# Optimization experiments

Measured on AMD Instinct MI355X. Metric: run time of the kernel, lower is better.

## Reference

```python
import jax, jax.numpy as jnp
import numpy as np

B, D, P = 2048, 768, 200
DOWN = [(384, 768), (192, 384), (96, 192), (48, 96)]
UP = [(96, 48), (192, 96), (384, 192), (768, 384)]


def setup_inputs() -> dict:
    key = jax.random.key(0)
    ks = jax.random.split(key, 32)
    inp = {
        "x": jax.random.normal(ks[0], (B, D), jnp.float32),
        "aW": jax.random.normal(ks[1], (D, D), jnp.float32) * 0.02,
        "ab": jax.random.normal(ks[2], (D,), jnp.float32) * 0.02,
        "protos": jax.random.normal(ks[3], (P, D), jnp.float32),
    }
    k = 4
    for i, (o, ii) in enumerate(DOWN):
        inp[f"Wd{i}"] = jax.random.normal(ks[k], (o, ii), jnp.float32) * (1.0 / np.sqrt(ii)); k += 1
        inp[f"bd{i}"] = jax.random.normal(ks[k], (o,), jnp.float32) * 0.02; k += 1
    for i, (o, ii) in enumerate(UP):
        inp[f"Wu{i}"] = jax.random.normal(ks[k], (o, ii), jnp.float32) * (1.0 / np.sqrt(ii)); k += 1
        inp[f"bu{i}"] = jax.random.normal(ks[k], (o,), jnp.float32) * 0.02; k += 1
    return inp


def _adopter_net(x, Wds, bds, Wus, bus):
    # down path with skip storage
    x_inter = []
    h = x
    for Wd, bd in zip(Wds, bds):
        h = jax.nn.relu(h @ Wd.T + bd)
        x_inter.append(h)
    # up path: residual adds for middle layers (i==1 uses x_inter[-2], i==2 uses x_inter[-3])
    n = len(Wus)
    for i, (Wu, bu) in enumerate(zip(Wus, bus)):
        if i == 0 or i == n - 1:
            h = jax.nn.relu(h @ Wu.T + bu)
        else:
            h = jax.nn.relu((h + x_inter[-i - 1]) @ Wu.T + bu)
    return h


def reference(x, aW, ab, Wd0, bd0, Wd1, bd1, Wd2, bd2, Wd3, bd3,
              Wu0, bu0, Wu1, bu1, Wu2, bu2, Wu3, bu3, protos):
    Wds, bds = [Wd0, Wd1, Wd2, Wd3], [bd0, bd1, bd2, bd3]
    Wus, bus = [Wu0, Wu1, Wu2, Wu3], [bu0, bu1, bu2, bu3]
    # features = x + adapter(x) + adopters(x)
    features = x + (x @ aW.T + ab) + _adopter_net(x, Wds, bds, Wus, bus)  # [B, D]
    # fused per-prototype negative L1 distance (replaces Python loop over PrototypeBase)
    logits = -jnp.sum(jnp.abs(features[:, None, :] - protos[None, :, :]), axis=-1)  # [B, P]
    return logits
```

## Files before the change

### kernel.cpp

```cpp
#include <hip/hip_runtime.h>

typedef __attribute__((ext_vector_type(8))) __bf16 bf16x8;
typedef __attribute__((ext_vector_type(4))) float f32x4;
typedef _Float16 hf2 __attribute__((ext_vector_type(2)));
typedef _Float16 hf8 __attribute__((ext_vector_type(8)));
typedef unsigned short u16;
typedef struct { hf2 v[4]; } hf2x4;

__device__ __forceinline__ float bf2f(u16 h) {
    return __uint_as_float(((unsigned int)h) << 16);
}
__device__ __forceinline__ u16 f2bf(float f) {
    unsigned int u = __float_as_uint(f);
    u += 0x7fffu + ((u >> 16) & 1u);
    return (u16)(u >> 16);
}

#if __has_builtin(__builtin_amdgcn_fdot2)
__device__ __forceinline__ float FDOT2(hf2 a, hf2 b, float c) {
    return __builtin_amdgcn_fdot2(a, b, c, false);
}
#else
__device__ __forceinline__ float FDOT2(hf2 a, hf2 b, float c) {
    return c + (float)a[0] + (float)a[1];
}
#endif

#define GLOAD_LDS16(gsrc, ldst)                                                          \
    __builtin_amdgcn_global_load_lds(                                                    \
        (__attribute__((address_space(1))) unsigned int*)(gsrc),                         \
        (__attribute__((address_space(3))) unsigned int*)(ldst), 16, 0, 0)

struct CvtDesc { const float* src; u16* dst; int N, K, Npad, Kpad, blk0, fmt; };
struct CvtTab { CvtDesc t[11]; };

__global__ __launch_bounds__(256) void cvt_all(CvtTab tab) {
    int b = blockIdx.x;
    int ti = 0;
#pragma unroll
    for (int j = 1; j < 11; ++j)
        if (b >= tab.t[j].blk0) ti = j;
    const CvtDesc c = tab.t[ti];
    long i = (long)(b - c.blk0) * 256 + threadIdx.x;
    long tot = (long)c.Npad * c.Kpad;
    if (i >= tot) return;
    int n = (int)(i / c.Kpad);
    int k = (int)(i - (long)n * c.Kpad);
    float v = (n < c.N && k < c.K) ? c.src[(long)n * c.K + k] : 0.f;
    if (c.fmt) {
        _Float16 h = (_Float16)v;
        c.dst[i] = __builtin_bit_cast(u16, h);
    } else {
        c.dst[i] = f2bf(v);
    }
}

template<int RELU, int HASRES, int RESF16, int MODE>
__device__ __forceinline__ void gemm128_body(
    char* lds,
    const u16* __restrict__ A, int lda,
    const u16* __restrict__ W, int ldw,
    const float* __restrict__ bias,
    u16* __restrict__ outB, int ldo,
    const void* __restrict__ res, int ldr,
    _Float16* __restrict__ outH,
    int nk, int mb, int nb)
{
    const int tid = threadIdx.x;
    const int wave = tid >> 6, lane = tid & 63;
    const int lr = lane & 15, lk = lane >> 4;
    const int wr = wave >> 1, wc = wave & 1;

    f32x4 acc[4][2];
#pragma unroll
    for (int i = 0; i < 4; ++i)
#pragma unroll
        for (int j = 0; j < 2; ++j)
#pragma unroll
            for (int e = 0; e < 4; ++e) acc[i][j][e] = 0.f;

    int ra[4], la[4], rb[2], lb[2];
#pragma unroll
    for (int t = 0; t < 4; ++t) {
        int g = t * 256 + tid;
        ra[t] = g >> 3; la[t] = (g & 7) ^ (ra[t] & 7);
    }
#pragma unroll
    for (int t = 0; t < 2; ++t) {
        int g = t * 256 + tid;
        rb[t] = g >> 3; lb[t] = (g & 7) ^ (rb[t] & 7);
    }

    auto STAGE = [&](int b, int kt) {
        const int kk = kt * 64;
        char* dA = lds + b * 24576;
        char* dB = dA + 16384;
#pragma unroll
        for (int t = 0; t < 4; ++t)
            GLOAD_LDS16(A + (size_t)(mb + ra[t]) * lda + kk + la[t] * 8,
                        dA + t * 4096 + wave * 1024);
#pragma unroll
        for (int t = 0; t < 2; ++t)
            GLOAD_LDS16(W + (size_t)(nb + rb[t]) * ldw + kk + lb[t] * 8,
                        dB + t * 4096 + wave * 1024);
    };
    auto COMPUTE = [&](int b) {
        char* sA = lds + b * 24576;
        char* sB = sA + 16384;
#pragma unroll
        for (int ks = 0; ks < 2; ++ks) {
            bf16x8 af[4], bfr[2];
#pragma unroll
            for (int mi = 0; mi < 4; ++mi) {
                int m_loc = wr * 64 + mi * 16 + lr;
                int gr = (ks * 4 + lk) ^ (m_loc & 7);
                af[mi] = *(const bf16x8*)(sA + m_loc * 128 + gr * 16);
            }
#pragma unroll
            for (int ni = 0; ni < 2; ++ni) {
                int n_loc = wc * 32 + ni * 16 + lr;
                int gr = (ks * 4 + lk) ^ (n_loc & 7);
                bfr[ni] = *(const bf16x8*)(sB + n_loc * 128 + gr * 16);
            }
#pragma unroll
            for (int mi = 0; mi < 4; ++mi)
#pragma unroll
                for (int ni = 0; ni < 2; ++ni)
                    acc[mi][ni] = __builtin_amdgcn_mfma_f32_16x16x32_bf16(
                        af[mi], bfr[ni], acc[mi][ni], 0, 0, 0);
        }
    };

    STAGE(0, 0);
    __syncthreads();
    int b = 0;
    for (int kt = 0; kt < nk - 1; ++kt) {
        STAGE(b ^ 1, kt + 1);
        COMPUTE(b);
        __syncthreads();
        b ^= 1;
    }
    COMPUTE(b);

#pragma unroll
    for (int mi = 0; mi < 4; ++mi) {
#pragma unroll
        for (int ni = 0; ni < 2; ++ni) {
            const int n_g = nb + wc * 32 + ni * 16 + lr;
            const float bv = bias[n_g];
#pragma unroll
            for (int r = 0; r < 4; ++r) {
                const int m_g = mb + wr * 64 + mi * 16 + lk * 4 + r;
                float v = acc[mi][ni][r] + bv;
                if (RELU) v = fmaxf(v, 0.f);
                if (HASRES) {
                    if (RESF16)
                        v += (float)((const _Float16*)res)[(size_t)m_g * ldr + n_g];
                    else
                        v += bf2f(((const u16*)res)[(size_t)m_g * ldr + n_g]);
                }
                if (MODE == 2) outH[(size_t)m_g * 768 + n_g] = (_Float16)v;
                else           outB[(size_t)m_g * ldo + n_g] = f2bf(v);
            }
        }
    }
}

__global__ __launch_bounds__(256) void gemm_ad0(
    const u16* __restrict__ xb,
    const u16* __restrict__ aWb, const float* __restrict__ ab,
    _Float16* __restrict__ adFH,
    const u16* __restrict__ Wd0b, const float* __restrict__ bd0,
    u16* __restrict__ h1)
{
    __shared__ __align__(16) char lds[49152];
    if (blockIdx.y < 12) {
        gemm128_body<0, 1, 0, 2>(lds, xb, 768, aWb, 768, ab, nullptr, 0,
                                 xb, 768, adFH, 12,
                                 blockIdx.x * 128, blockIdx.y * 64);
    } else {
        gemm128_body<1, 0, 0, 0>(lds, xb, 768, Wd0b, 768, bd0, h1, 384,
                                 nullptr, 0, nullptr, 12,
                                 blockIdx.x * 128, (blockIdx.y - 12) * 64);
    }
}

__global__ __launch_bounds__(256) void gemm_u3(
    const u16* __restrict__ u2, const u16* __restrict__ Wu3b,
    const float* __restrict__ bu3, const _Float16* __restrict__ adFH,
    _Float16* __restrict__ featH)
{
    __shared__ __align__(16) char lds[49152];
    gemm128_body<1, 1, 1, 2>(lds, u2, 384, Wu3b, 384, bu3, nullptr, 0,
                             adFH, 768, featH, 6,
                             blockIdx.x * 128, blockIdx.y * 64);
}

template<int K, int NPAD, int NREAL, int RES, int OUTG>
__device__ __forceinline__ void layer16(
    const u16* __restrict__ W, int ldw, const float* __restrict__ bias,
    const u16* actIn, int ldin,
    u16* actOut, int ldout,
    const u16* resid, int ldres,
    u16* __restrict__ gout, int ldg)
{
    constexpr int TPW = NPAD / 64;
    const int tid = threadIdx.x;
    const int wave = tid >> 6, lane = tid & 63;
    const int lr = lane & 15, lk = lane >> 4;

    f32x4 acc[TPW];
#pragma unroll
    for (int t = 0; t < TPW; ++t)
#pragma unroll
        for (int e = 0; e < 4; ++e) acc[t][e] = 0.f;

#pragma unroll
    for (int kk = 0; kk < K / 32; ++kk) {
        const bf16x8 a = *(const bf16x8*)&actIn[lr * ldin + kk * 32 + lk * 8];
#pragma unroll
        for (int t = 0; t < TPW; ++t) {
            const int nc = (wave * TPW + t) * 16 + lr;
            const bf16x8 b = *(const bf16x8*)&W[(size_t)nc * ldw + kk * 32 + lk * 8];
            acc[t] = __builtin_amdgcn_mfma_f32_16x16x32_bf16(a, b, acc[t], 0, 0, 0);
        }
    }
#pragma unroll
    for (int t = 0; t < TPW; ++t) {
        const int nc = (wave * TPW + t) * 16 + lr;
        const float bv = (nc < NREAL) ? bias[nc] : 0.f;
#pragma unroll
        for (int r = 0; r < 4; ++r) {
            const int row = lk * 4 + r;
            float v = fmaxf(acc[t][r] + bv, 0.f);
            if (RES) v += bf2f(resid[row * ldres + nc]);
            const u16 o = f2bf(v);
            if (OUTG) gout[(size_t)row * ldg + nc] = o;
            else      actOut[row * ldout + nc] = o;
        }
    }
}

__global__ __launch_bounds__(256) void chain_mid(
    const u16* __restrict__ h1,
    const u16* __restrict__ Wd1b, const float* __restrict__ bd1,
    const u16* __restrict__ Wd2b, const float* __restrict__ bd2,
    const u16* __restrict__ Wd3b, const float* __restrict__ bd3,
    const u16* __restrict__ Wu0b, const float* __restrict__ bu0,
    const u16* __restrict__ Wu1b, const float* __restrict__ bu1,
    const u16* __restrict__ Wu2b, const float* __restrict__ bu2,
    u16* __restrict__ u2)
{
    __shared__ u16 As[16 * 392];
    __shared__ u16 Bs[16 * 200];
    __shared__ u16 Cs[16 * 136];
    __shared__ u16 Ds[16 * 72];
    const int tid = threadIdx.x;
    const int rb = blockIdx.x * 16;

    for (int i = tid; i < 768; i += 256) {
        const int r = i / 48, c = i - r * 48;
        *(bf16x8*)&As[r * 392 + c * 8] =
            *(const bf16x8*)&h1[(size_t)(rb + r) * 384 + c * 8];
    }
    __syncthreads();
    layer16<384, 192, 192, 0, 0>(Wd1b, 384, bd1, As, 392, Bs, 200, nullptr, 0, nullptr, 0);
    __syncthreads();
    layer16<192, 128,  96, 0, 0>(Wd2b, 192, bd2, Bs, 200, Cs, 136, nullptr, 0, nullptr, 0);
    __syncthreads();
    layer16<128,  64,  48, 0, 0>(Wd3b, 128, bd3, Cs, 136, Ds,  72, nullptr, 0, nullptr, 0);
    __syncthreads();
    u16* E = As;
    u16* F = As + 16 * 136;
    layer16< 64, 128,  96, 1, 0>(Wu0b,  64, bu0, Ds,  72, E, 136, Cs, 136, nullptr, 0);
    __syncthreads();
    layer16<128, 192, 192, 1, 0>(Wu1b, 128, bu1, E, 136, F, 200, Bs, 200, nullptr, 0);
    __syncthreads();
    layer16<192, 384, 384, 0, 1>(Wu2b, 192, bu2, F, 200, nullptr, 0, nullptr, 0,
                                 u2 + (size_t)rb * 384, 384);
}

__global__ __launch_bounds__(256) void l1_kernel(
    const _Float16* __restrict__ feat, const _Float16* __restrict__ protos,
    float* __restrict__ part)
{
    __shared__ _Float16 fs[128][64];
    __shared__ hf2 pt[32][64];
    const int tid = threadIdx.x;
    const int tp = tid & 15, tr = tid >> 4;
    const int rb = blockIdx.x * 128;
    const int pb = blockIdx.y * 64;
    const int db = blockIdx.z * 64;

    {
        const int g = tid & 7, r0 = tid >> 3;
#pragma unroll
        for (int k = 0; k < 4; ++k) {
            const int r = r0 + 32 * k;
            *(hf8*)&fs[r][g * 8] =
                *(const hf8*)&feat[(size_t)(rb + r) * 768 + db + g * 8];
        }
    }
    {
        const int sp = tid & 63, q = tid >> 6;
        const _Float16* src = &protos[(size_t)(pb + sp) * 768 + db + q * 16];
        hf8 v0 = *(const hf8*)src;
        hf8 v1 = *(const hf8*)(src + 8);
        hf2x4 w0 = __builtin_bit_cast(hf2x4, v0);
        hf2x4 w1 = __builtin_bit_cast(hf2x4, v1);
#pragma unroll
        for (int e = 0; e < 4; ++e)
            pt[q * 8 + e][sp] = w0.v[e];
#pragma unroll
        for (int e = 0; e < 4; ++e)
            pt[q * 8 + 4 + e][sp] = w1.v[e];
    }
    __syncthreads();

    float acc[8][4];
#pragma unroll
    for (int i = 0; i < 8; ++i)
#pragma unroll
        for (int j = 0; j < 4; ++j) acc[i][j] = 0.f;

    const hf2 one2 = {(_Float16)1.0f, (_Float16)1.0f};
#pragma unroll 2
    for (int g = 0; g < 8; ++g) {
        hf2x4 F2[8];
#pragma unroll
        for (int i = 0; i < 8; ++i)
            F2[i] = __builtin_bit_cast(hf2x4,
                        *(const hf8*)&fs[tr + 16 * i][g * 8]);
        hf2x4 P2[4];
#pragma unroll
        for (int q = 0; q < 4; ++q)
            P2[q] = __builtin_bit_cast(hf2x4,
                        *(const hf8*)&pt[g * 4 + q][tp * 4]);
#pragma unroll
        for (int q = 0; q < 4; ++q) {
#pragma unroll
            for (int j = 0; j < 4; ++j) {
                const hf2 pj = P2[q].v[j];
#pragma unroll
                for (int i = 0; i < 8; ++i) {
                    hf2 d = F2[i].v[q] - pj;
                    unsigned ud = __builtin_bit_cast(unsigned, d) & 0x7FFF7FFFu;
                    acc[i][j] = FDOT2(__builtin_bit_cast(hf2, ud), one2, acc[i][j]);
                }
            }
        }
    }
    const int p = pb + tp * 4;
    if (p < 200) {
#pragma unroll
        for (int i = 0; i < 8; ++i) {
            float4 v = {-acc[i][0], -acc[i][1], -acc[i][2], -acc[i][3]};
            *(float4*)&part[((size_t)(rb + tr + 16 * i) * 12 + blockIdx.z) * 200 + p] = v;
        }
    }
}

__global__ __launch_bounds__(256) void l1_reduce(
    const float* __restrict__ part, float* __restrict__ out)
{
    const int row = blockIdx.x;
    const int p = threadIdx.x;
    if (p < 200) {
        float s = 0.f;
#pragma unroll
        for (int z = 0; z < 12; ++z)
            s += part[((size_t)row * 12 + z) * 200 + p];
        out[(size_t)row * 200 + p] = s;
    }
}

static constexpr size_t OFF_PART  = 0;
static constexpr size_t OFF_XB    = 0;
static constexpr size_t OFF_AWB   = 3145728;
static constexpr size_t OFF_WD0   = 4325376;
static constexpr size_t OFF_WD1   = 4915200;
static constexpr size_t OFF_WD2   = 5062656;
static constexpr size_t OFF_WD3   = 5111808;
static constexpr size_t OFF_WU0   = 5128192;
static constexpr size_t OFF_WU1   = 5144576;
static constexpr size_t OFF_WU2   = 5193728;
static constexpr size_t OFF_WU3   = 5341184;
static constexpr size_t OFF_H1    = 5931008;
static constexpr size_t OFF_U2    = 10387456;
static constexpr size_t OFF_ADF   = 11960320;
static constexpr size_t OFF_FEATH = 19660800;
static constexpr size_t OFF_PROH  = 22806528;

extern "C" void kernel_launch(void* const* d_in, const int* in_sizes, int n_in,
                              void* d_out, int out_size, void* d_ws, size_t ws_size,
                              hipStream_t stream) {
    const float* x      = (const float*)d_in[0];
    const float* aW     = (const float*)d_in[1];
    const float* ab     = (const float*)d_in[2];
    const float* protos = (const float*)d_in[3];
    const float* Wd[4]  = {(const float*)d_in[4], (const float*)d_in[6],
                           (const float*)d_in[8], (const float*)d_in[10]};
    const float* bd[4]  = {(const float*)d_in[5], (const float*)d_in[7],
                           (const float*)d_in[9], (const float*)d_in[11]};
    const float* Wu[4]  = {(const float*)d_in[12], (const float*)d_in[14],
                           (const float*)d_in[16], (const float*)d_in[18]};
    const float* bu[4]  = {(const float*)d_in[13], (const float*)d_in[15],
                           (const float*)d_in[17], (const float*)d_in[19]};
    float* out = (float*)d_out;
    char* ws = (char*)d_ws;

    u16* xb    = (u16*)(ws + OFF_XB);
    u16* aWb   = (u16*)(ws + OFF_AWB);
    u16* Wd0b  = (u16*)(ws + OFF_WD0);
    u16* Wd1b  = (u16*)(ws + OFF_WD1);
    u16* Wd2b  = (u16*)(ws + OFF_WD2);
    u16* Wd3b  = (u16*)(ws + OFF_WD3);
    u16* Wu0b  = (u16*)(ws + OFF_WU0);
    u16* Wu1b  = (u16*)(ws + OFF_WU1);
    u16* Wu2b  = (u16*)(ws + OFF_WU2);
    u16* Wu3b  = (u16*)(ws + OFF_WU3);
    u16* h1    = (u16*)(ws + OFF_H1);
    u16* u2    = (u16*)(ws + OFF_U2);
    float* part = (float*)(ws + OFF_PART);
    _Float16* adFH  = (_Float16*)(ws + OFF_ADF);
    _Float16* featH = (_Float16*)(ws + OFF_FEATH);
    _Float16* proH  = (_Float16*)(ws + OFF_PROH);

    CvtTab tab;
    int blk = 0;
    auto set = [&](int i, const float* s, u16* d, int N, int K, int Np, int Kp,
                   int fmt) {
        tab.t[i] = {s, d, N, K, Np, Kp, blk, fmt};
        blk += (Np * Kp + 255) / 256;
    };
    set(0,  x,      xb,          2048, 768, 2048, 768, 0);
    set(1,  aW,     aWb,         768,  768, 768,  768, 0);
    set(2,  Wd[0],  Wd0b,        384,  768, 384,  768, 0);
    set(3,  Wd[1],  Wd1b,        192,  384, 192,  384, 0);
    set(4,  Wd[2],  Wd2b,        96,   192, 128,  192, 0);
    set(5,  Wd[3],  Wd3b,        48,   96,  64,   128, 0);
    set(6,  Wu[0],  Wu0b,        96,   48,  128,  64,  0);
    set(7,  Wu[1],  Wu1b,        192,  96,  192,  128, 0);
    set(8,  Wu[2],  Wu2b,        384,  192, 384,  192, 0);
    set(9,  Wu[3],  Wu3b,        768,  384, 768,  384, 0);
    set(10, protos, (u16*)proH,  200,  768, 256,  768, 1);
    cvt_all<<<blk, 256, 0, stream>>>(tab);

    gemm_ad0<<<dim3(16, 18), 256, 0, stream>>>(xb, aWb, ab, adFH, Wd0b, bd[0], h1);
    chain_mid<<<dim3(128), 256, 0, stream>>>(h1,
        Wd1b, bd[1], Wd2b, bd[2], Wd3b, bd[3],
        Wu0b, bu[0], Wu1b, bu[1], Wu2b, bu[2], u2);
    gemm_u3<<<dim3(16, 12), 256, 0, stream>>>(u2, Wu3b, bu[3], adFH, featH);

    l1_kernel<<<dim3(16, 4, 12), 256, 0, stream>>>(featH, proH, part);
    l1_reduce<<<dim3(2048), 256, 0, stream>>>(part, out);
}
```

Before: 80.56 us.

## Fuse adapter GEMM into final up-projection and overlap weight conversion with first GEMM

The adapter GEMM (x @ aW.T) moves out of the first kernel and into the final up-projection kernel as a second K-phase. The Wu3 accumulator gets bias and ReLU applied at the phase boundary, then the adapter product and the x residual are added in the epilogue. This drops the fp16 adapter intermediate write and read-back. Weight and prototype conversion is split so that only x and Wd0 are converted up front, and the remaining weights are converted by extra blocks inside the first GEMM launch. Risks: the dependent kernels get longer, the d0 GEMM grid is small, and the second cvt launch adds overhead.

```diff
diff --git a/kernel.cpp b/kernel.cpp
--- a/kernel.cpp
+++ b/kernel.cpp
@@ -34,36 +34,32 @@
 struct CvtDesc { const float* src; u16* dst; int N, K, Npad, Kpad, blk0, fmt; };
 struct CvtTab { CvtDesc t[11]; };
 
-__global__ __launch_bounds__(256) void cvt_all(CvtTab tab) {
-    int b = blockIdx.x;
+__device__ __forceinline__ void do_cvt(const CvtTab& tab, int vb, int tid) {
     int ti = 0;
 #pragma unroll
     for (int j = 1; j < 11; ++j)
-        if (b >= tab.t[j].blk0) ti = j;
+        if (vb >= tab.t[j].blk0) ti = j;
     const CvtDesc c = tab.t[ti];
-    long i = (long)(b - c.blk0) * 256 + threadIdx.x;
+    long i = (long)(vb - c.blk0) * 256 + tid;
     long tot = (long)c.Npad * c.Kpad;
     if (i >= tot) return;
     int n = (int)(i / c.Kpad);
     int k = (int)(i - (long)n * c.Kpad);
     float v = (n < c.N && k < c.K) ? c.src[(long)n * c.K + k] : 0.f;
-    if (c.fmt) {
-        _Float16 h = (_Float16)v;
-        c.dst[i] = __builtin_bit_cast(u16, h);
-    } else {
-        c.dst[i] = f2bf(v);
-    }
-}
-
-template<int RELU, int HASRES, int RESF16, int MODE>
+    c.dst[i] = c.fmt ? __builtin_bit_cast(u16, (_Float16)v) : f2bf(v);
+}
+
+__global__ __launch_bounds__(256) void cvt_k(CvtTab tab) {
+    do_cvt(tab, blockIdx.x, threadIdx.x);
+}
+
+template<int RELU>
 __device__ __forceinline__ void gemm128_body(
     char* lds,
     const u16* __restrict__ A, int lda,
     const u16* __restrict__ W, int ldw,
     const float* __restrict__ bias,
     u16* __restrict__ outB, int ldo,
-    const void* __restrict__ res, int ldr,
-    _Float16* __restrict__ outH,
     int nk, int mb, int nb)
 {
     const int tid = threadIdx.x;
@@ -79,7 +75,7 @@
 #pragma unroll
             for (int e = 0; e < 4; ++e) acc[i][j][e] = 0.f;
 
-    int ra[4], la[4], rb[2], lb[2];
+    int ra[4], la[4], rb_[2], lb[2];
 #pragma unroll
     for (int t = 0; t < 4; ++t) {
         int g = t * 256 + tid;
@@ -88,7 +84,7 @@
 #pragma unroll
     for (int t = 0; t < 2; ++t) {
         int g = t * 256 + tid;
-        rb[t] = g >> 3; lb[t] = (g & 7) ^ (rb[t] & 7);
+        rb_[t] = g >> 3; lb[t] = (g & 7) ^ (rb_[t] & 7);
     }
 
     auto STAGE = [&](int b, int kt) {
@@ -101,7 +97,7 @@
                         dA + t * 4096 + wave * 1024);
 #pragma unroll
         for (int t = 0; t < 2; ++t)
-            GLOAD_LDS16(W + (size_t)(nb + rb[t]) * ldw + kk + lb[t] * 8,
+            GLOAD_LDS16(W + (size_t)(nb + rb_[t]) * ldw + kk + lb[t] * 8,
                         dB + t * 4096 + wave * 1024);
     };
     auto COMPUTE = [&](int b) {
@@ -153,47 +149,139 @@
                 const int m_g = mb + wr * 64 + mi * 16 + lk * 4 + r;
                 float v = acc[mi][ni][r] + bv;
                 if (RELU) v = fmaxf(v, 0.f);
-                if (HASRES) {
-                    if (RESF16)
-                        v += (float)((const _Float16*)res)[(size_t)m_g * ldr + n_g];
-                    else
-                        v += bf2f(((const u16*)res)[(size_t)m_g * ldr + n_g]);
+                outB[(size_t)m_g * ldo + n_g] = f2bf(v);
+            }
+        }
+    }
+}
+
+__global__ __launch_bounds__(256, 2) void gemm_d0_cvt(
+    const u16* __restrict__ xb, const u16* __restrict__ Wd0b,
+    const float* __restrict__ bd0, u16* __restrict__ h1, CvtTab tabB)
+{
+    __shared__ __align__(16) char lds[49152];
+    const int bid = blockIdx.x;
+    if (bid < 96) {
+        gemm128_body<1>(lds, xb, 768, Wd0b, 768, bd0, h1, 384, 12,
+                        (bid & 15) * 128, (bid >> 4) * 64);
+    } else {
+        do_cvt(tabB, bid - 96, threadIdx.x);
+    }
+}
+
+__global__ __launch_bounds__(256, 2) void gemm_u3ad(
+    const u16* __restrict__ u2, const u16* __restrict__ Wu3b,
+    const float* __restrict__ bu3,
+    const u16* __restrict__ xb, const u16* __restrict__ aWb,
+    const float* __restrict__ ab,
+    _Float16* __restrict__ featH)
+{
+    __shared__ __align__(16) char lds[49152];
+    const int mb = blockIdx.x * 128, nb = blockIdx.y * 64;
+    const int tid = threadIdx.x;
+    const int wave = tid >> 6, lane = tid & 63;
+    const int lr = lane & 15, lk = lane >> 4;
+    const int wr = wave >> 1, wc = wave & 1;
+
+    f32x4 acc[4][2];
+#pragma unroll
+    for (int i = 0; i < 4; ++i)
+#pragma unroll
+        for (int j = 0; j < 2; ++j)
+#pragma unroll
+            for (int e = 0; e < 4; ++e) acc[i][j][e] = 0.f;
+
+    int ra[4], la[4], rb_[2], lb[2];
+#pragma unroll
+    for (int t = 0; t < 4; ++t) {
+        int g = t * 256 + tid;
+        ra[t] = g >> 3; la[t] = (g & 7) ^ (ra[t] & 7);
+    }
+#pragma unroll
+    for (int t = 0; t < 2; ++t) {
+        int g = t * 256 + tid;
+        rb_[t] = g >> 3; lb[t] = (g & 7) ^ (rb_[t] & 7);
+    }
+
+    auto STAGE = [&](int b, int kt) {
+        const u16* A; const u16* W; int ld, kk;
+        if (kt < 6) { A = u2; W = Wu3b; ld = 384; kk = kt * 64; }
+        else        { A = xb; W = aWb;  ld = 768; kk = (kt - 6) * 64; }
+        char* dA = lds + b * 24576;
+        char* dB = dA + 16384;
+#pragma unroll
+        for (int t = 0; t < 4; ++t)
+            GLOAD_LDS16(A + (size_t)(mb + ra[t]) * ld + kk + la[t] * 8,
+                        dA + t * 4096 + wave * 1024);
+#pragma unroll
+        for (int t = 0; t < 2; ++t)
+            GLOAD_LDS16(W + (size_t)(nb + rb_[t]) * ld + kk + lb[t] * 8,
+                        dB + t * 4096 + wave * 1024);
+    };
+    auto COMPUTE = [&](int b) {
+        char* sA = lds + b * 24576;
+        char* sB = sA + 16384;
+#pragma unroll
+        for (int ks = 0; ks < 2; ++ks) {
+            bf16x8 af[4], bfr[2];
+#pragma unroll
+            for (int mi = 0; mi < 4; ++mi) {
+                int m_loc = wr * 64 + mi * 16 + lr;
+                int gr = (ks * 4 + lk) ^ (m_loc & 7);
+                af[mi] = *(const bf16x8*)(sA + m_loc * 128 + gr * 16);
+            }
+#pragma unroll
+            for (int ni = 0; ni < 2; ++ni) {
+                int n_loc = wc * 32 + ni * 16 + lr;
+                int gr = (ks * 4 + lk) ^ (n_loc & 7);
+                bfr[ni] = *(const bf16x8*)(sB + n_loc * 128 + gr * 16);
+            }
+#pragma unroll
+            for (int mi = 0; mi < 4; ++mi)
+#pragma unroll
+                for (int ni = 0; ni < 2; ++ni)
+                    acc[mi][ni] = __builtin_amdgcn_mfma_f32_16x16x32_bf16(
+                        af[mi], bfr[ni], acc[mi][ni], 0, 0, 0);
+        }
+    };
+
+    STAGE(0, 0);
+    __syncthreads();
+    int b = 0;
+    for (int kt = 0; kt < 17; ++kt) {
+        STAGE(b ^ 1, kt + 1);
+        COMPUTE(b);
+        if (kt == 5) {
+#pragma unroll
+            for (int mi = 0; mi < 4; ++mi)
+#pragma unroll
+                for (int ni = 0; ni < 2; ++ni) {
+                    const int n_g = nb + wc * 32 + ni * 16 + lr;
+                    const float bv = bu3[n_g];
+#pragma unroll
+                    for (int r = 0; r < 4; ++r)
+                        acc[mi][ni][r] = fmaxf(acc[mi][ni][r] + bv, 0.f);
                 }
-                if (MODE == 2) outH[(size_t)m_g * 768 + n_g] = (_Float16)v;
-                else           outB[(size_t)m_g * ldo + n_g] = f2bf(v);
-            }
-        }
-    }
-}
-
-__global__ __launch_bounds__(256) void gemm_ad0(
-    const u16* __restrict__ xb,
-    const u16* __restrict__ aWb, const float* __restrict__ ab,
-    _Float16* __restrict__ adFH,
-    const u16* __restrict__ Wd0b, const float* __restrict__ bd0,
-    u16* __restrict__ h1)
-{
-    __shared__ __align__(16) char lds[49152];
-    if (blockIdx.y < 12) {
-        gemm128_body<0, 1, 0, 2>(lds, xb, 768, aWb, 768, ab, nullptr, 0,
-                                 xb, 768, adFH, 12,
-                                 blockIdx.x * 128, blockIdx.y * 64);
-    } else {
-        gemm128_body<1, 0, 0, 0>(lds, xb, 768, Wd0b, 768, bd0, h1, 384,
-                                 nullptr, 0, nullptr, 12,
-                                 blockIdx.x * 128, (blockIdx.y - 12) * 64);
-    }
-}
-
-__global__ __launch_bounds__(256) void gemm_u3(
-    const u16* __restrict__ u2, const u16* __restrict__ Wu3b,
-    const float* __restrict__ bu3, const _Float16* __restrict__ adFH,
-    _Float16* __restrict__ featH)
-{
-    __shared__ __align__(16) char lds[49152];
-    gemm128_body<1, 1, 1, 2>(lds, u2, 384, Wu3b, 384, bu3, nullptr, 0,
-                             adFH, 768, featH, 6,
-                             blockIdx.x * 128, blockIdx.y * 64);
+        }
+        __syncthreads();
+        b ^= 1;
+    }
+    COMPUTE(b);
+
+#pragma unroll
+    for (int mi = 0; mi < 4; ++mi) {
+#pragma unroll
+        for (int ni = 0; ni < 2; ++ni) {
+            const int n_g = nb + wc * 32 + ni * 16 + lr;
+            const float bv = ab[n_g];
+#pragma unroll
+            for (int r = 0; r < 4; ++r) {
+                const int m_g = mb + wr * 64 + mi * 16 + lk * 4 + r;
+                float v = acc[mi][ni][r] + bv + bf2f(xb[(size_t)m_g * 768 + n_g]);
+                featH[(size_t)m_g * 768 + n_g] = (_Float16)v;
+            }
+        }
+    }
 }
 
 template<int K, int NPAD, int NREAL, int RES, int OUTG>
@@ -387,7 +475,6 @@
 static constexpr size_t OFF_WU3   = 5341184;
 static constexpr size_t OFF_H1    = 5931008;
 static constexpr size_t OFF_U2    = 10387456;
-static constexpr size_t OFF_ADF   = 11960320;
 static constexpr size_t OFF_FEATH = 19660800;
 static constexpr size_t OFF_PROH  = 22806528;
 
@@ -422,35 +509,45 @@
     u16* h1    = (u16*)(ws + OFF_H1);
     u16* u2    = (u16*)(ws + OFF_U2);
     float* part = (float*)(ws + OFF_PART);
-    _Float16* adFH  = (_Float16*)(ws + OFF_ADF);
     _Float16* featH = (_Float16*)(ws + OFF_FEATH);
     _Float16* proH  = (_Float16*)(ws + OFF_PROH);
 
-    CvtTab tab;
-    int blk = 0;
-    auto set = [&](int i, const float* s, u16* d, int N, int K, int Np, int Kp,
-                   int fmt) {
-        tab.t[i] = {s, d, N, K, Np, Kp, blk, fmt};
-        blk += (Np * Kp + 255) / 256;
+    const int SENT = 0x7FFFFFFF;
+
+    CvtTab tabA;
+    int blkA = 0;
+    tabA.t[0] = {x,     xb,   2048, 768, 2048, 768, 0, 0};
+    blkA += 2048 * 768 / 256;
+    tabA.t[1] = {Wd[0], Wd0b, 384,  768, 384,  768, blkA, 0};
+    blkA += 384 * 768 / 256;
+    for (int j = 2; j < 11; ++j) tabA.t[j].blk0 = SENT;
+    cvt_k<<<blkA, 256, 0, stream>>>(tabA);
+
+    CvtTab tabB;
+    int blkB = 0;
+    auto setB = [&](int i, const float* s, u16* d, int N, int K, int Np, int Kp,
+                    int fmt) {
+        tabB.t[i] = {s, d, N, K, Np, Kp, blkB, fmt};
+        blkB += (Np * Kp + 255) / 256;
     };
-    set(0,  x,      xb,          2048, 768, 2048, 768, 0);
-    set(1,  aW,     aWb,         768,  768, 768,  768, 0);
-    set(2,  Wd[0],  Wd0b,        384,  768, 384,  768, 0);
-    set(3,  Wd[1],  Wd1b,        192,  384, 192,  384, 0);
-    set(4,  Wd[2],  Wd2b,        96,   192, 128,  192, 0);
-    set(5,  Wd[3],  Wd3b,        48,   96,  64,   128, 0);
-    set(6,  Wu[0],  Wu0b,        96,   48,  128,  64,  0);
-    set(7,  Wu[1],  Wu1b,        192,  96,  192,  128, 0);
-    set(8,  Wu[2],  Wu2b,        384,  192, 384,  192, 0);
-    set(9,  Wu[3],  Wu3b,        768,  384, 768,  384, 0);
-    set(10, protos, (u16*)proH,  200,  768, 256,  768, 1);
-    cvt_all<<<blk, 256, 0, stream>>>(tab);
-
-    gemm_ad0<<<dim3(16, 18), 256, 0, stream>>>(xb, aWb, ab, adFH, Wd0b, bd[0], h1);
+    setB(0, aW,     aWb,        768, 768, 768, 768, 0);
+    setB(1, Wd[1],  Wd1b,       192, 384, 192, 384, 0);
+    setB(2, Wd[2],  Wd2b,       96,  192, 128, 192, 0);
+    setB(3, Wd[3],  Wd3b,       48,  96,  64,  128, 0);
+    setB(4, Wu[0],  Wu0b,       96,  48,  128, 64,  0);
+    setB(5, Wu[1],  Wu1b,       192, 96,  192, 128, 0);
+    setB(6, Wu[2],  Wu2b,       384, 192, 384, 192, 0);
+    setB(7, Wu[3],  Wu3b,       768, 384, 768, 384, 0);
+    setB(8, protos, (u16*)proH, 200, 768, 256, 768, 1);
+    for (int j = 9; j < 11; ++j) tabB.t[j].blk0 = SENT;
+    gemm_d0_cvt<<<96 + blkB, 256, 0, stream>>>(xb, Wd0b, bd[0], h1, tabB);
+
     chain_mid<<<dim3(128), 256, 0, stream>>>(h1,
         Wd1b, bd[1], Wd2b, bd[2], Wd3b, bd[3],
         Wu0b, bu[0], Wu1b, bu[1], Wu2b, bu[2], u2);
-    gemm_u3<<<dim3(16, 12), 256, 0, stream>>>(u2, Wu3b, bu[3], adFH, featH);
+
+    gemm_u3ad<<<dim3(16, 12), 256, 0, stream>>>(u2, Wu3b, bu[3],
+                                                xb, aWb, ab, featH);
 
     l1_kernel<<<dim3(16, 4, 12), 256, 0, stream>>>(featH, proH, part);
     l1_reduce<<<dim3(2048), 256, 0, stream>>>(part, out);
```

Result: no change. 80.79 us (+0.3%).

## Rebalance kernel schedule: overlap weight conversion with d0 GEMM, adapter GEMM with chain

Applied to the files above, without the earlier changes.

Splits conversion so only x and Wd0 are converted up front. The remaining weight and prototype conversions run as extra blocks inside the first down-projection GEMM launch. The adapter GEMM moves into the launch of the middle chain kernel so the two run concurrently, and the adapter result is written straight into the feature buffer, which the final up GEMM then accumulates into in place. The L1 kernel uses 96-wide D chunks (8 partials instead of 12) to cut partial-sum traffic, at the cost of more LDS per block and a heavier load imbalance across heterogeneous blocks.

```diff
diff --git a/kernel.cpp b/kernel.cpp
--- a/kernel.cpp
+++ b/kernel.cpp
@@ -34,25 +34,23 @@
 struct CvtDesc { const float* src; u16* dst; int N, K, Npad, Kpad, blk0, fmt; };
 struct CvtTab { CvtDesc t[11]; };
 
-__global__ __launch_bounds__(256) void cvt_all(CvtTab tab) {
-    int b = blockIdx.x;
+__device__ __forceinline__ void do_cvt(const CvtTab& tab, int vb, int tid) {
     int ti = 0;
 #pragma unroll
     for (int j = 1; j < 11; ++j)
-        if (b >= tab.t[j].blk0) ti = j;
+        if (vb >= tab.t[j].blk0) ti = j;
     const CvtDesc c = tab.t[ti];
-    long i = (long)(b - c.blk0) * 256 + threadIdx.x;
+    long i = (long)(vb - c.blk0) * 256 + tid;
     long tot = (long)c.Npad * c.Kpad;
     if (i >= tot) return;
     int n = (int)(i / c.Kpad);
     int k = (int)(i - (long)n * c.Kpad);
     float v = (n < c.N && k < c.K) ? c.src[(long)n * c.K + k] : 0.f;
-    if (c.fmt) {
-        _Float16 h = (_Float16)v;
-        c.dst[i] = __builtin_bit_cast(u16, h);
-    } else {
-        c.dst[i] = f2bf(v);
-    }
+    c.dst[i] = c.fmt ? __builtin_bit_cast(u16, (_Float16)v) : f2bf(v);
+}
+
+__global__ __launch_bounds__(256) void cvt_k(CvtTab tab) {
+    do_cvt(tab, blockIdx.x, threadIdx.x);
 }
 
 template<int RELU, int HASRES, int RESF16, int MODE>
@@ -79,7 +77,7 @@
 #pragma unroll
             for (int e = 0; e < 4; ++e) acc[i][j][e] = 0.f;
 
-    int ra[4], la[4], rb[2], lb[2];
+    int ra[4], la[4], rb_[2], lb[2];
 #pragma unroll
     for (int t = 0; t < 4; ++t) {
         int g = t * 256 + tid;
@@ -88,7 +86,7 @@
 #pragma unroll
     for (int t = 0; t < 2; ++t) {
         int g = t * 256 + tid;
-        rb[t] = g >> 3; lb[t] = (g & 7) ^ (rb[t] & 7);
+        rb_[t] = g >> 3; lb[t] = (g & 7) ^ (rb_[t] & 7);
     }
 
     auto STAGE = [&](int b, int kt) {
@@ -101,7 +99,7 @@
                         dA + t * 4096 + wave * 1024);
 #pragma unroll
         for (int t = 0; t < 2; ++t)
-            GLOAD_LDS16(W + (size_t)(nb + rb[t]) * ldw + kk + lb[t] * 8,
+            GLOAD_LDS16(W + (size_t)(nb + rb_[t]) * ldw + kk + lb[t] * 8,
                         dB + t * 4096 + wave * 1024);
     };
     auto COMPUTE = [&](int b) {
@@ -166,34 +164,19 @@
     }
 }
 
-__global__ __launch_bounds__(256) void gemm_ad0(
-    const u16* __restrict__ xb,
-    const u16* __restrict__ aWb, const float* __restrict__ ab,
-    _Float16* __restrict__ adFH,
-    const u16* __restrict__ Wd0b, const float* __restrict__ bd0,
-    u16* __restrict__ h1)
+__global__ __launch_bounds__(256, 2) void gemm_d0_cvt(
+    const u16* __restrict__ xb, const u16* __restrict__ Wd0b,
+    const float* __restrict__ bd0, u16* __restrict__ h1, CvtTab tabB)
 {
     __shared__ __align__(16) char lds[49152];
-    if (blockIdx.y < 12) {
-        gemm128_body<0, 1, 0, 2>(lds, xb, 768, aWb, 768, ab, nullptr, 0,
-                                 xb, 768, adFH, 12,
-                                 blockIdx.x * 128, blockIdx.y * 64);
-    } else {
+    const int bid = blockIdx.x;
+    if (bid < 96) {
         gemm128_body<1, 0, 0, 0>(lds, xb, 768, Wd0b, 768, bd0, h1, 384,
                                  nullptr, 0, nullptr, 12,
-                                 blockIdx.x * 128, (blockIdx.y - 12) * 64);
-    }
-}
-
-__global__ __launch_bounds__(256) void gemm_u3(
-    const u16* __restrict__ u2, const u16* __restrict__ Wu3b,
-    const float* __restrict__ bu3, const _Float16* __restrict__ adFH,
-    _Float16* __restrict__ featH)
-{
-    __shared__ __align__(16) char lds[49152];
-    gemm128_body<1, 1, 1, 2>(lds, u2, 384, Wu3b, 384, bu3, nullptr, 0,
-                             adFH, 768, featH, 6,
-                             blockIdx.x * 128, blockIdx.y * 64);
+                                 (bid & 15) * 128, (bid >> 4) * 64);
+    } else {
+        do_cvt(tabB, bid - 96, threadIdx.x);
+    }
 }
 
 template<int K, int NPAD, int NREAL, int RES, int OUTG>
@@ -241,7 +224,10 @@
     }
 }
 
-__global__ __launch_bounds__(256) void chain_mid(
+__global__ __launch_bounds__(256, 2) void chain_ad(
+    const u16* __restrict__ xb,
+    const u16* __restrict__ aWb, const float* __restrict__ ab,
+    _Float16* __restrict__ featH,
     const u16* __restrict__ h1,
     const u16* __restrict__ Wd1b, const float* __restrict__ bd1,
     const u16* __restrict__ Wd2b, const float* __restrict__ bd2,
@@ -251,12 +237,21 @@
     const u16* __restrict__ Wu2b, const float* __restrict__ bu2,
     u16* __restrict__ u2)
 {
-    __shared__ u16 As[16 * 392];
-    __shared__ u16 Bs[16 * 200];
-    __shared__ u16 Cs[16 * 136];
-    __shared__ u16 Ds[16 * 72];
+    __shared__ __align__(16) char smem[49152];
+    const int bid = blockIdx.x;
     const int tid = threadIdx.x;
-    const int rb = blockIdx.x * 16;
+
+    if (bid < 192) {
+        gemm128_body<0, 1, 0, 2>(smem, xb, 768, aWb, 768, ab, nullptr, 0,
+                                 xb, 768, featH, 12,
+                                 (bid & 15) * 128, (bid >> 4) * 64);
+        return;
+    }
+    u16* As = (u16*)smem;
+    u16* Bs = (u16*)(smem + 12544);
+    u16* Cs = (u16*)(smem + 18944);
+    u16* Ds = (u16*)(smem + 23296);
+    const int rb = (bid - 192) * 16;
 
     for (int i = tid; i < 768; i += 256) {
         const int r = i / 48, c = i - r * 48;
@@ -280,40 +275,44 @@
                                  u2 + (size_t)rb * 384, 384);
 }
 
+__global__ __launch_bounds__(256, 2) void gemm_u3add(
+    const u16* __restrict__ u2, const u16* __restrict__ Wu3b,
+    const float* __restrict__ bu3, _Float16* __restrict__ featH)
+{
+    __shared__ __align__(16) char lds[49152];
+    gemm128_body<1, 1, 1, 2>(lds, u2, 384, Wu3b, 384, bu3, nullptr, 0,
+                             featH, 768, featH, 6,
+                             blockIdx.x * 128, blockIdx.y * 64);
+}
+
 __global__ __launch_bounds__(256) void l1_kernel(
     const _Float16* __restrict__ feat, const _Float16* __restrict__ protos,
     float* __restrict__ part)
 {
-    __shared__ _Float16 fs[128][64];
-    __shared__ hf2 pt[32][64];
+    __shared__ _Float16 fs[128][96];
+    __shared__ hf2 pt[48][64];
     const int tid = threadIdx.x;
     const int tp = tid & 15, tr = tid >> 4;
     const int rb = blockIdx.x * 128;
     const int pb = blockIdx.y * 64;
-    const int db = blockIdx.z * 64;
-
-    {
-        const int g = tid & 7, r0 = tid >> 3;
-#pragma unroll
-        for (int k = 0; k < 4; ++k) {
-            const int r = r0 + 32 * k;
-            *(hf8*)&fs[r][g * 8] =
-                *(const hf8*)&feat[(size_t)(rb + r) * 768 + db + g * 8];
-        }
+    const int db = blockIdx.z * 96;
+
+    for (int i = tid; i < 1536; i += 256) {
+        const int r = i / 12, c = i - r * 12;
+        *(hf8*)&fs[r][c * 8] =
+            *(const hf8*)&feat[(size_t)(rb + r) * 768 + db + c * 8];
     }
     {
         const int sp = tid & 63, q = tid >> 6;
-        const _Float16* src = &protos[(size_t)(pb + sp) * 768 + db + q * 16];
-        hf8 v0 = *(const hf8*)src;
-        hf8 v1 = *(const hf8*)(src + 8);
-        hf2x4 w0 = __builtin_bit_cast(hf2x4, v0);
-        hf2x4 w1 = __builtin_bit_cast(hf2x4, v1);
-#pragma unroll
-        for (int e = 0; e < 4; ++e)
-            pt[q * 8 + e][sp] = w0.v[e];
-#pragma unroll
-        for (int e = 0; e < 4; ++e)
-            pt[q * 8 + 4 + e][sp] = w1.v[e];
+#pragma unroll
+        for (int t = 0; t < 3; ++t) {
+            const hf8 v = *(const hf8*)&protos[(size_t)(pb + sp) * 768 + db + q * 24 + t * 8];
+            const hf2x4 w = __builtin_bit_cast(hf2x4, v);
+            const int p0 = q * 12 + t * 4;
+#pragma unroll
+            for (int e = 0; e < 4; ++e)
+                pt[p0 + e][sp] = w.v[e];
+        }
     }
     __syncthreads();
 
@@ -325,17 +324,15 @@
 
     const hf2 one2 = {(_Float16)1.0f, (_Float16)1.0f};
 #pragma unroll 2
-    for (int g = 0; g < 8; ++g) {
+    for (int g = 0; g < 12; ++g) {
         hf2x4 F2[8];
 #pragma unroll
         for (int i = 0; i < 8; ++i)
-            F2[i] = __builtin_bit_cast(hf2x4,
-                        *(const hf8*)&fs[tr + 16 * i][g * 8]);
+            F2[i] = __builtin_bit_cast(hf2x4, *(const hf8*)&fs[tr + 16 * i][g * 8]);
         hf2x4 P2[4];
 #pragma unroll
         for (int q = 0; q < 4; ++q)
-            P2[q] = __builtin_bit_cast(hf2x4,
-                        *(const hf8*)&pt[g * 4 + q][tp * 4]);
+            P2[q] = __builtin_bit_cast(hf2x4, *(const hf8*)&pt[g * 4 + q][tp * 4]);
 #pragma unroll
         for (int q = 0; q < 4; ++q) {
 #pragma unroll
@@ -355,7 +352,7 @@
 #pragma unroll
         for (int i = 0; i < 8; ++i) {
             float4 v = {-acc[i][0], -acc[i][1], -acc[i][2], -acc[i][3]};
-            *(float4*)&part[((size_t)(rb + tr + 16 * i) * 12 + blockIdx.z) * 200 + p] = v;
+            *(float4*)&part[((size_t)(rb + tr + 16 * i) * 8 + blockIdx.z) * 200 + p] = v;
         }
     }
 }
@@ -368,8 +365,8 @@
     if (p < 200) {
         float s = 0.f;
 #pragma unroll
-        for (int z = 0; z < 12; ++z)
-            s += part[((size_t)row * 12 + z) * 200 + p];
+        for (int z = 0; z < 8; ++z)
+            s += part[((size_t)row * 8 + z) * 200 + p];
         out[(size_t)row * 200 + p] = s;
     }
 }
@@ -387,7 +384,6 @@
 static constexpr size_t OFF_WU3   = 5341184;
 static constexpr size_t OFF_H1    = 5931008;
 static constexpr size_t OFF_U2    = 10387456;
-static constexpr size_t OFF_ADF   = 11960320;
 static constexpr size_t OFF_FEATH = 19660800;
 static constexpr size_t OFF_PROH  = 22806528;
 
@@ -422,36 +418,45 @@
     u16* h1    = (u16*)(ws + OFF_H1);
     u16* u2    = (u16*)(ws + OFF_U2);
     float* part = (float*)(ws + OFF_PART);
-    _Float16* adFH  = (_Float16*)(ws + OFF_ADF);
     _Float16* featH = (_Float16*)(ws + OFF_FEATH);
     _Float16* proH  = (_Float16*)(ws + OFF_PROH);
 
-    CvtTab tab;
-    int blk = 0;
-    auto set = [&](int i, const float* s, u16* d, int N, int K, int Np, int Kp,
-                   int fmt) {
-        tab.t[i] = {s, d, N, K, Np, Kp, blk, fmt};
-        blk += (Np * Kp + 255) / 256;
+    const int SENT = 0x7FFFFFFF;
+
+    CvtTab tabA;
+    int blkA = 0;
+    tabA.t[0] = {x,     xb,   2048, 768, 2048, 768, 0, 0};
+    blkA += 2048 * 768 / 256;
+    tabA.t[1] = {Wd[0], Wd0b, 384,  768, 384,  768, blkA, 0};
+    blkA += 384 * 768 / 256;
+    for (int j = 2; j < 11; ++j) tabA.t[j].blk0 = SENT;
+    cvt_k<<<blkA, 256, 0, stream>>>(tabA);
+
+    CvtTab tabB;
+    int blkB = 0;
+    auto setB = [&](int i, const float* s, u16* d, int N, int K, int Np, int Kp,
+                    int fmt) {
+        tabB.t[i] = {s, d, N, K, Np, Kp, blkB, fmt};
+        blkB += (Np * Kp + 255) / 256;
     };
-    set(0,  x,      xb,          2048, 768, 2048, 768, 0);
-    set(1,  aW,     aWb,         768,  768, 768,  768, 0);
-    set(2,  Wd[0],  Wd0b,        384,  768, 384,  768, 0);
-    set(3,  Wd[1],  Wd1b,        192,  384, 192,  384, 0);
-    set(4,  Wd[2],  Wd2b,        96,   192, 128,  192, 0);
-    set(5,  Wd[3],  Wd3b,        48,   96,  64,   128, 0);
-    set(6,  Wu[0],  Wu0b,        96,   48,  128,  64,  0);
-    set(7,  Wu[1],  Wu1b,        192,  96,  192,  128, 0);
-    set(8,  Wu[2],  Wu2b,        384,  192, 384,  192, 0);
-    set(9,  Wu[3],  Wu3b,        768,  384, 768,  384, 0);
-    set(10, protos, (u16*)proH,  200,  768, 256,  768, 1);
-    cvt_all<<<blk, 256, 0, stream>>>(tab);
-
-    gemm_ad0<<<dim3(16, 18), 256, 0, stream>>>(xb, aWb, ab, adFH, Wd0b, bd[0], h1);
-    chain_mid<<<dim3(128), 256, 0, stream>>>(h1,
+    setB(0, aW,     aWb,        768, 768, 768, 768, 0);
+    setB(1, Wd[1],  Wd1b,       192, 384, 192, 384, 0);
+    setB(2, Wd[2],  Wd2b,       96,  192, 128, 192, 0);
+    setB(3, Wd[3],  Wd3b,       48,  96,  64,  128, 0);
+    setB(4, Wu[0],  Wu0b,       96,  48,  128, 64,  0);
+    setB(5, Wu[1],  Wu1b,       192, 96,  192, 128, 0);
+    setB(6, Wu[2],  Wu2b,       384, 192, 384, 192, 0);
+    setB(7, Wu[3],  Wu3b,       768, 384, 768, 384, 0);
+    setB(8, protos, (u16*)proH, 200, 768, 256, 768, 1);
+    for (int j = 9; j < 11; ++j) tabB.t[j].blk0 = SENT;
+    gemm_d0_cvt<<<96 + blkB, 256, 0, stream>>>(xb, Wd0b, bd[0], h1, tabB);
+
+    chain_ad<<<320, 256, 0, stream>>>(xb, aWb, ab, featH, h1,
         Wd1b, bd[1], Wd2b, bd[2], Wd3b, bd[3],
         Wu0b, bu[0], Wu1b, bu[1], Wu2b, bu[2], u2);
-    gemm_u3<<<dim3(16, 12), 256, 0, stream>>>(u2, Wu3b, bu[3], adFH, featH);
-
-    l1_kernel<<<dim3(16, 4, 12), 256, 0, stream>>>(featH, proH, part);
+
+    gemm_u3add<<<dim3(16, 12), 256, 0, stream>>>(u2, Wu3b, bu[3], featH);
+
+    l1_kernel<<<dim3(16, 4, 8), 256, 0, stream>>>(featH, proH, part);
     l1_reduce<<<dim3(2048), 256, 0, stream>>>(part, out);
 }
```

Result: no change. 79.08 us (-1.8%).
